# Kernel optimization log

Hardware: AMD Instinct MI355X
Metric: run time of the kernel (lower is better)

Reference implementation:

```python
import jax, jax.numpy as jnp
import numpy as np

# dims: N nodes, E edges, C channel multiplicity, NS species, RB radial basis, H radial mlp hidden
N, E, C, NS, RB, H = 4000, 128000, 128, 5, 8, 64
AVG_N = 32.0  # avg_n_neighbors


def setup_inputs() -> dict:
    key = jax.random.key(0)
    ks = jax.random.split(key, 17)
    return {
        "x_scalars": jax.random.normal(ks[0], (N, C), jnp.float32),
        "x_vectors": jax.random.normal(ks[1], (N, C, 3), jnp.float32),
        "edge_vectors": jax.random.normal(ks[2], (E, 3), jnp.float32) * 2.0,
        "radial_basis": jax.random.normal(ks[3], (E, RB), jnp.float32),
        "W1_0": jax.random.normal(ks[4], (C, C), jnp.float32),
        "W1_1": jax.random.normal(ks[5], (C, C), jnp.float32),
        "rmlp_w0": jax.random.normal(ks[6], (RB, H), jnp.float32) * np.float32(np.sqrt(4.0 / RB)),
        "rmlp_w1": jax.random.normal(ks[7], (H, H), jnp.float32) * np.float32(np.sqrt(4.0 / H)),
        "rmlp_w2": jax.random.normal(ks[8], (H, H), jnp.float32) * np.float32(np.sqrt(4.0 / H)),
        "rmlp_w3": jax.random.normal(ks[9], (H, 4 * C), jnp.float32) * np.float32(np.sqrt(1.0 / H)),
        "W2_0": jax.random.normal(ks[10], (2 * C, 2 * C), jnp.float32),
        "W2_1": jax.random.normal(ks[11], (2 * C, C), jnp.float32),
        "Wsk0": jax.random.normal(ks[12], (NS, C, 2 * C), jnp.float32),
        "Wsk1": jax.random.normal(ks[13], (NS, C, C), jnp.float32),
        "species": jax.random.randint(ks[14], (N,), 0, NS),
        "senders": jax.random.randint(ks[15], (E,), 0, N),
        "receivers": jax.random.randint(ks[16], (E,), 0, N),
    }


def reference(x_scalars, x_vectors, edge_vectors, radial_basis,
              W1_0, W1_1, rmlp_w0, rmlp_w1, rmlp_w2, rmlp_w3,
              W2_0, W2_1, Wsk0, Wsk1, species, senders, receivers):
    n_nodes = x_scalars.shape[0]
    inv_c = 1.0 / jnp.sqrt(jnp.float32(C))
    # linear_1: per-irrep channel mixing (e3nn path-normalized Linear)
    y0 = (x_scalars @ W1_0) * inv_c                                  # [N,C] 0e
    y1 = jnp.einsum('nci,cd->ndi', x_vectors, W1_1) * inv_c          # [N,C,3] 1o
    # gather to edges
    m0 = y0[senders]                                                 # [E,C]
    m1 = y1[senders]                                                 # [E,C,3]
    # spherical harmonics lmax=1, component normalization: Y0=1, Y1=sqrt(3)*unit_vec
    r = jnp.linalg.norm(edge_vectors, axis=1, keepdims=True)
    u = edge_vectors / jnp.maximum(r, 1e-12)
    Y1 = jnp.sqrt(3.0) * u                                           # [E,3]
    # tensor product filtered to 0e,1o (explicit Clebsch-Gordan, component norm)
    t0a = m0                                                         # 0e x 0e -> 0e
    t0b = jnp.einsum('eci,ei->ec', m1, Y1) / jnp.sqrt(3.0)           # 1o x 1o -> 0e
    t1a = m0[:, :, None] * Y1[:, None, :]                            # 0e x 1o -> 1o
    t1b = m1                                                         # 1o x 0e -> 1o
    # radial MLP (silu, no bias), one scalar weight per tp irrep (4C total)
    h = jax.nn.silu(radial_basis @ rmlp_w0)
    h = jax.nn.silu(h @ rmlp_w1)
    h = jax.nn.silu(h @ rmlp_w2)
    w = h @ rmlp_w3                                                  # [E,4C]
    ws0, ws1 = w[:, :C], w[:, C:2 * C]
    wv0, wv1 = w[:, 2 * C:3 * C], w[:, 3 * C:]
    scal = jnp.concatenate([t0a * ws0, t0b * ws1], axis=1)           # [E,2C]
    vec = jnp.concatenate([t1a * wv0[:, :, None], t1b * wv1[:, :, None]], axis=1)  # [E,2C,3]
    # scatter-add to receivers, neighbor normalization
    inv_nb = 1.0 / jnp.sqrt(jnp.float32(AVG_N))
    agg_s = jax.ops.segment_sum(scal, receivers, num_segments=n_nodes) * inv_nb
    agg_v = jax.ops.segment_sum(vec, receivers, num_segments=n_nodes) * inv_nb
    # linear_2: tp irreps -> (2C)x0e + Cx1o  (C output scalars + C gates)
    inv_2c = 1.0 / jnp.sqrt(jnp.float32(2 * C))
    s = (agg_s @ W2_0) * inv_2c                                      # [N,2C]
    v = jnp.einsum('nci,cd->ndi', agg_v, W2_1) * inv_2c              # [N,C,3]
    # indexed (per-species) skip connection
    s = s + jnp.einsum('nc,ncd->nd', x_scalars, Wsk0[species]) * inv_c
    v = v + jnp.einsum('nci,ncd->ndi', x_vectors, Wsk1[species]) * inv_c
    # gate: silu on scalars, silu(gates) multiplies 1o features
    out_s = jax.nn.silu(s[:, :C])
    gates = jax.nn.silu(s[:, C:])
    out_v = v * gates[:, :, None]
    return jnp.concatenate([out_s, out_v.reshape(n_nodes, 3 * C)], axis=1)  # [N,4C]
```

## Files before the change

kernel.cpp:

```cpp
#include <hip/hip_runtime.h>
#include <math.h>

#define CC 128
#define HH 64
#define RBD 8
#define WDIM 512

typedef __attribute__((ext_vector_type(8))) short short8v;
typedef __attribute__((ext_vector_type(4))) float f32x4;

__device__ __forceinline__ float silu_f(float x) {
    return x / (1.0f + __expf(-x));
}

__device__ __forceinline__ unsigned short f2bf(float x) {
    unsigned int b = __float_as_uint(x);
    unsigned int r = (b + 0x7FFFu + ((b >> 16) & 1u)) >> 16;
    return (unsigned short)r;
}

__device__ __forceinline__ float bf2f(unsigned short u) {
    return __uint_as_float(((unsigned int)u) << 16);
}

__global__ void k_prep(const float* __restrict__ w0, const float* __restrict__ w1,
                       const float* __restrict__ w2, const float* __restrict__ w3,
                       float* __restrict__ w0T, float* __restrict__ w1T,
                       float* __restrict__ w2T, float* __restrict__ w3T,
                       unsigned short* __restrict__ w3bs,
                       unsigned short* __restrict__ w0b,
                       unsigned short* __restrict__ w1b,
                       unsigned short* __restrict__ w2b) {
    int i = blockIdx.x * blockDim.x + threadIdx.x;
    if (i < 64 * 8) { int m = i / 8, k = i % 8; w0T[i] = w0[k * 64 + m]; }
    if (i < 64 * 64) { int m = i / 64, k = i % 64; w1T[i] = w1[k * 64 + m]; w2T[i] = w2[k * 64 + m]; }
    if (i < 512 * 64) { int j = i / 64, k = i % 64; w3T[i] = w3[k * 512 + j]; }
    if (i < 32768) {
        int t = i >> 10, ch = (i >> 9) & 1, lane = (i >> 3) & 63, j = i & 7;
        int k = ch * 32 + 8 * (lane >> 4) + j;
        int n = t * 16 + (lane & 15);
        w3bs[i] = f2bf(w3[k * 512 + n]);
    }
    if (i < 2048) {
        int t = i >> 9, lane = (i >> 3) & 63, j = i & 7;
        int k = 8 * (lane >> 4) + j;
        int col = t * 16 + (lane & 15);
        w0b[i] = (k < RBD) ? f2bf(w0[k * 64 + col]) : (unsigned short)0;
    }
    if (i < 4096) {
        int f = i >> 9, lane = (i >> 3) & 63, j = i & 7;
        int ks = f >> 2, t = f & 3;
        int k = ks * 32 + 8 * (lane >> 4) + j;
        int col = t * 16 + (lane & 15);
        w1b[i] = f2bf(w1[k * 64 + col]);
        w2b[i] = f2bf(w2[k * 64 + col]);
    }
}

__global__ void k_hist(const int* __restrict__ rcv, int* __restrict__ deg, int E_) {
    int e = blockIdx.x * blockDim.x + threadIdx.x;
    if (e < E_) atomicAdd(&deg[rcv[e]], 1);
}

__global__ __launch_bounds__(1024) void k_scan(const int* __restrict__ deg,
                                               int* __restrict__ off, int N) {
    __shared__ int s[1024];
    int t = threadIdx.x;
    int b = t * 4;
    int a0 = (b + 0 < N) ? deg[b + 0] : 0;
    int a1 = (b + 1 < N) ? deg[b + 1] : 0;
    int a2 = (b + 2 < N) ? deg[b + 2] : 0;
    int a3 = (b + 3 < N) ? deg[b + 3] : 0;
    int part = a0 + a1 + a2 + a3;
    s[t] = part;
    __syncthreads();
    for (int d = 1; d < 1024; d <<= 1) {
        int v = (t >= d) ? s[t - d] : 0;
        __syncthreads();
        s[t] += v;
        __syncthreads();
    }
    int excl = s[t] - part;
    if (b + 0 <= N) off[b + 0] = excl;
    if (b + 1 <= N) off[b + 1] = excl + a0;
    if (b + 2 <= N) off[b + 2] = excl + a0 + a1;
    if (b + 3 <= N) off[b + 3] = excl + a0 + a1 + a2;
}

__global__ void k_scatter(const int* __restrict__ rcv, const int* __restrict__ off,
                          int* __restrict__ cur, int* __restrict__ elist, int E_) {
    int e = blockIdx.x * blockDim.x + threadIdx.x;
    if (e < E_) {
        int r = rcv[e];
        int p = atomicAdd(&cur[r], 1);
        elist[off[r] + p] = e;
    }
}

__global__ void k_emeta(const int* __restrict__ elist, const int* __restrict__ snd,
                        const float* __restrict__ evec,
                        float4* __restrict__ up, int* __restrict__ sp, int E_) {
    int p = blockIdx.x * blockDim.x + threadIdx.x;
    if (p >= E_) return;
    int e = elist[p];
    float e0 = evec[(size_t)e * 3 + 0];
    float e1 = evec[(size_t)e * 3 + 1];
    float e2 = evec[(size_t)e * 3 + 2];
    float rn = sqrtf(e0 * e0 + e1 * e1 + e2 * e2);
    float inv = 1.0f / fmaxf(rn, 1e-12f);
    up[p] = make_float4(e0 * inv, e1 * inv, e2 * inv, 0.f);
    sp[p] = snd[e];
}

__global__ __launch_bounds__(128) void k_node_lin(
    const float* __restrict__ xs, const float* __restrict__ xv,
    const float* __restrict__ W10, const float* __restrict__ W11,
    float* __restrict__ y0, float* __restrict__ y1, int N) {
    const int d = threadIdx.x;
    const int n0 = blockIdx.x * 4;
    const int NP = N * CC;
    const float inv_c = 0.08838834764831845f;
    float a0[4] = {0.f, 0.f, 0.f, 0.f};
    float av[4][3] = {};
    #pragma unroll 4
    for (int c = 0; c < CC; c++) {
        float w10 = W10[c * CC + d];
        float w11 = W11[c * CC + d];
        #pragma unroll
        for (int n = 0; n < 4; n++) {
            a0[n] += xs[(n0 + n) * CC + c] * w10;
            #pragma unroll
            for (int i = 0; i < 3; i++)
                av[n][i] += xv[((n0 + n) * CC + c) * 3 + i] * w11;
        }
    }
    #pragma unroll
    for (int n = 0; n < 4; n++) {
        y0[(n0 + n) * CC + d] = a0[n] * inv_c;
        #pragma unroll
        for (int i = 0; i < 3; i++)
            y1[i * NP + (n0 + n) * CC + d] = av[n][i] * inv_c;
    }
}

__device__ __forceinline__ void layer64(const float4* a, float4* b,
                                        const float* __restrict__ W) {
    #pragma unroll
    for (int m = 0; m < 16; m++) {
        float s0 = 0.f, s1 = 0.f, s2 = 0.f, s3 = 0.f;
        const float* w0p = W + (4 * m + 0) * 64;
        const float* w1p = W + (4 * m + 1) * 64;
        const float* w2p = W + (4 * m + 2) * 64;
        const float* w3p = W + (4 * m + 3) * 64;
        #pragma unroll
        for (int k = 0; k < 16; k++) {
            float4 av = a[k];
            s0 += av.x * w0p[4 * k + 0] + av.y * w0p[4 * k + 1] + av.z * w0p[4 * k + 2] + av.w * w0p[4 * k + 3];
            s1 += av.x * w1p[4 * k + 0] + av.y * w1p[4 * k + 1] + av.z * w1p[4 * k + 2] + av.w * w1p[4 * k + 3];
            s2 += av.x * w2p[4 * k + 0] + av.y * w2p[4 * k + 1] + av.z * w2p[4 * k + 2] + av.w * w2p[4 * k + 3];
            s3 += av.x * w3p[4 * k + 0] + av.y * w3p[4 * k + 1] + av.z * w3p[4 * k + 2] + av.w * w3p[4 * k + 3];
        }
        b[m] = make_float4(silu_f(s0), silu_f(s1), silu_f(s2), silu_f(s3));
    }
}

__device__ __forceinline__ void mlp_body(
    const float* __restrict__ rb, int e,
    const float* __restrict__ w0T, const float* __restrict__ w1T,
    const float* __restrict__ w2T, float4* a) {
    float rbv[RBD];
    #pragma unroll
    for (int k = 0; k < RBD; k++) rbv[k] = rb[(size_t)e * RBD + k];
    float4 b[16];
    #pragma unroll
    for (int m = 0; m < 16; m++) {
        float s0 = 0.f, s1 = 0.f, s2 = 0.f, s3 = 0.f;
        #pragma unroll
        for (int k = 0; k < RBD; k++) {
            float rv = rbv[k];
            s0 += rv * w0T[(4 * m + 0) * RBD + k];
            s1 += rv * w0T[(4 * m + 1) * RBD + k];
            s2 += rv * w0T[(4 * m + 2) * RBD + k];
            s3 += rv * w0T[(4 * m + 3) * RBD + k];
        }
        a[m] = make_float4(silu_f(s0), silu_f(s1), silu_f(s2), silu_f(s3));
    }
    layer64(a, b, w1T);
    layer64(b, a, w2T);
}

__global__ __launch_bounds__(256) void k_mlpw3(
    const float* __restrict__ rb, const int* __restrict__ elist,
    const unsigned short* __restrict__ w0b, const unsigned short* __restrict__ w1b,
    const unsigned short* __restrict__ w2b, const unsigned short* __restrict__ w3bs,
    unsigned int* __restrict__ Wq, int E_) {
    const int lane = threadIdx.x & 63;
    const int wv = threadIdx.x >> 6;
    const int rbk = blockIdx.x * 4 + wv;
    const int col = lane & 15;
    const int grp = lane >> 4;

    __shared__ unsigned short hbuf[4][16][72];

    short8v a0 = (short8v){0, 0, 0, 0, 0, 0, 0, 0};
    if (grp == 0) {
        int e = elist[rbk * 16 + col];
        const float* rp = rb + (size_t)e * RBD;
        #pragma unroll
        for (int j = 0; j < RBD; j++) a0[j] = (short)f2bf(rp[j]);
    }
    f32x4 acc[4];
    {
        const unsigned short* bp = w0b + (size_t)lane * 8;
        #pragma unroll
        for (int t = 0; t < 4; t++) {
            short8v b = *(const short8v*)(bp + (size_t)t * 512);
            acc[t] = __builtin_amdgcn_mfma_f32_16x16x32_bf16(
                a0, b, (f32x4){0.f, 0.f, 0.f, 0.f}, 0, 0, 0);
        }
    }
    #pragma unroll
    for (int t = 0; t < 4; t++)
        #pragma unroll
        for (int r = 0; r < 4; r++)
            hbuf[wv][grp * 4 + r][t * 16 + col] = f2bf(silu_f(acc[t][r]));
    __syncthreads();

    {
        short8v aA = *(const short8v*)&hbuf[wv][col][8 * grp];
        short8v aB = *(const short8v*)&hbuf[wv][col][32 + 8 * grp];
        const unsigned short* bp = w1b + (size_t)lane * 8;
        #pragma unroll
        for (int t = 0; t < 4; t++) {
            short8v b0 = *(const short8v*)(bp + (size_t)(0 + t) * 512);
            short8v b1 = *(const short8v*)(bp + (size_t)(4 + t) * 512);
            f32x4 c = __builtin_amdgcn_mfma_f32_16x16x32_bf16(
                aA, b0, (f32x4){0.f, 0.f, 0.f, 0.f}, 0, 0, 0);
            acc[t] = __builtin_amdgcn_mfma_f32_16x16x32_bf16(aB, b1, c, 0, 0, 0);
        }
    }
    __syncthreads();
    #pragma unroll
    for (int t = 0; t < 4; t++)
        #pragma unroll
        for (int r = 0; r < 4; r++)
            hbuf[wv][grp * 4 + r][t * 16 + col] = f2bf(silu_f(acc[t][r]));
    __syncthreads();

    {
        short8v aA = *(const short8v*)&hbuf[wv][col][8 * grp];
        short8v aB = *(const short8v*)&hbuf[wv][col][32 + 8 * grp];
        const unsigned short* bp = w2b + (size_t)lane * 8;
        #pragma unroll
        for (int t = 0; t < 4; t++) {
            short8v b0 = *(const short8v*)(bp + (size_t)(0 + t) * 512);
            short8v b1 = *(const short8v*)(bp + (size_t)(4 + t) * 512);
            f32x4 c = __builtin_amdgcn_mfma_f32_16x16x32_bf16(
                aA, b0, (f32x4){0.f, 0.f, 0.f, 0.f}, 0, 0, 0);
            acc[t] = __builtin_amdgcn_mfma_f32_16x16x32_bf16(aB, b1, c, 0, 0, 0);
        }
    }
    __syncthreads();
    #pragma unroll
    for (int t = 0; t < 4; t++)
        #pragma unroll
        for (int r = 0; r < 4; r++)
            hbuf[wv][grp * 4 + r][t * 16 + col] = f2bf(silu_f(acc[t][r]));
    __syncthreads();

    short8v A0 = *(const short8v*)&hbuf[wv][col][8 * grp];
    short8v A1 = *(const short8v*)&hbuf[wv][col][32 + 8 * grp];

    f32x4 wacc[32];
    #pragma unroll
    for (int t = 0; t < 32; t++) wacc[t] = (f32x4){0.f, 0.f, 0.f, 0.f};

    const unsigned short* bbase = w3bs + (size_t)lane * 8;
    #pragma unroll
    for (int t = 0; t < 32; t++) {
        short8v b0 = *(const short8v*)(bbase + (size_t)(t * 2 + 0) * 512);
        short8v b1 = *(const short8v*)(bbase + (size_t)(t * 2 + 1) * 512);
        wacc[t] = __builtin_amdgcn_mfma_f32_16x16x32_bf16(A0, b0, wacc[t], 0, 0, 0);
        wacc[t] = __builtin_amdgcn_mfma_f32_16x16x32_bf16(A1, b1, wacc[t], 0, 0, 0);
    }

    const int rowq = grp * 4;
    const int jbase = rbk * 16 + rowq;
    #pragma unroll
    for (int t = 0; t < 16; t++) {
        #pragma unroll
        for (int rr = 0; rr < 4; rr++) {
            unsigned lo = f2bf(wacc[t][rr]);
            unsigned hi = f2bf(wacc[t + 16][rr]);
            Wq[(size_t)(jbase + rr) * 256 + t * 16 + col] = lo | (hi << 16);
        }
    }
}

__global__ __launch_bounds__(256, 4) void k_gather_em(
    const int* __restrict__ off, const float4* __restrict__ up,
    const int* __restrict__ sp, const unsigned int* __restrict__ Wq,
    const float* __restrict__ y0, const float* __restrict__ y1, int NP,
    float* __restrict__ agg_s, float* __restrict__ agg_v) {
    const int r = blockIdx.x;
    const int tid = threadIdx.x;
    const int half = tid >> 7;
    const int c = tid & 127;
    const int start = off[r];
    const int end = off[r + 1];

    float accs = 0.f, av0 = 0.f, av1 = 0.f, av2 = 0.f;
    const float SQ3 = 1.7320508075688772f;

    #pragma unroll 2
    for (int j = start; j < end; j++) {
        unsigned wq = Wq[(size_t)j * 256 + tid];
        float4 u = up[j];
        int s = __builtin_amdgcn_readfirstlane(sp[j]);
        float wa = bf2f((unsigned short)(wq & 0xFFFFu));
        float wb = bf2f((unsigned short)(wq >> 16));
        if (half == 0) {
            float f = y0[(size_t)s * CC + c];
            accs += f * wa;
            float bb = f * wb * SQ3;
            av0 += bb * u.x; av1 += bb * u.y; av2 += bb * u.z;
        } else {
            float f0 = y1[0 * NP + s * CC + c];
            float f1 = y1[1 * NP + s * CC + c];
            float f2 = y1[2 * NP + s * CC + c];
            accs += (f0 * u.x + f1 * u.y + f2 * u.z) * wa;
            av0 += f0 * wb; av1 += f1 * wb; av2 += f2 * wb;
        }
    }

    agg_s[(size_t)r * 256 + tid] = accs;
    float* o = agg_v + ((size_t)r * 256 + tid) * 3;
    o[0] = av0; o[1] = av1; o[2] = av2;
}

__global__ __launch_bounds__(256) void k_mlp_wp(
    const float* __restrict__ rb, const int* __restrict__ elist,
    const float* __restrict__ w0T, const float* __restrict__ w1T,
    const float* __restrict__ w2T, const float* __restrict__ w3T,
    unsigned short* __restrict__ Wp, int E_) {
    int p = blockIdx.x * blockDim.x + threadIdx.x;
    if (p >= E_) return;
    int e = elist[p];
    const int c0 = blockIdx.y * 128;

    float4 a[16];
    mlp_body(rb, e, w0T, w1T, w2T, a);

    const size_t E4 = (size_t)E_ * 4;
    for (int c = c0; c < c0 + 128; c += 8) {
        float s[8];
        #pragma unroll
        for (int q = 0; q < 8; q++) {
            const float* rp = w3T + (size_t)(c + q) * 64;
            float t0 = 0.f, t1 = 0.f, t2 = 0.f, t3 = 0.f;
            #pragma unroll
            for (int k = 0; k < 16; k++) {
                float4 h = a[k];
                t0 += h.x * rp[4 * k + 0];
                t1 += h.y * rp[4 * k + 1];
                t2 += h.z * rp[4 * k + 2];
                t3 += h.w * rp[4 * k + 3];
            }
            s[q] = (t0 + t1) + (t2 + t3);
        }
        ushort4 pk0 = make_ushort4(f2bf(s[0]), f2bf(s[1]), f2bf(s[2]), f2bf(s[3]));
        ushort4 pk1 = make_ushort4(f2bf(s[4]), f2bf(s[5]), f2bf(s[6]), f2bf(s[7]));
        *(ushort4*)(Wp + (size_t)(c >> 2) * E4 + (size_t)p * 4) = pk0;
        *(ushort4*)(Wp + (size_t)((c >> 2) + 1) * E4 + (size_t)p * 4) = pk1;
    }
}

__global__ __launch_bounds__(512, 2) void k_gather_wg(
    const int* __restrict__ off, const int* __restrict__ elist,
    const int* __restrict__ snd, const float* __restrict__ evec,
    const unsigned short* __restrict__ Wp, int E_,
    const float* __restrict__ y0, const float* __restrict__ y1, int NP,
    float* __restrict__ agg_s, float* __restrict__ agg_v) {
    const int r = blockIdx.x;
    const int tid = threadIdx.x;
    const int part = tid >> 7;
    const int c = tid & 127;

    const int start = off[r];
    const int end = off[r + 1];

    const unsigned short* __restrict__ wstream =
        Wp + (size_t)(tid >> 2) * ((size_t)E_ * 4) + (tid & 3);

    float acc0 = 0.f, acc1 = 0.f, acc2 = 0.f;
    const float SQ3 = 1.7320508075688772f;

    #pragma unroll 2
    for (int j = start; j < end; j++) {
        int e = elist[j];
        e = __builtin_amdgcn_readfirstlane(e);
        int s = snd[e];
        s = __builtin_amdgcn_readfirstlane(s);

        float e0 = evec[(size_t)e * 3 + 0];
        float e1 = evec[(size_t)e * 3 + 1];
        float e2 = evec[(size_t)e * 3 + 2];
        float rn = sqrtf(e0 * e0 + e1 * e1 + e2 * e2);
        float inv = 1.0f / fmaxf(rn, 1e-12f);
        float ux = e0 * inv, uy = e1 * inv, uz = e2 * inv;

        float w = bf2f(wstream[(size_t)j * 4]);

        if (part == 0) {
            acc0 += y0[(size_t)s * CC + c] * w;
        } else if (part == 1) {
            float f = y1[0 * NP + s * CC + c] * ux
                    + y1[1 * NP + s * CC + c] * uy
                    + y1[2 * NP + s * CC + c] * uz;
            acc0 += f * w;
        } else if (part == 2) {
            float bb = y0[(size_t)s * CC + c] * w * SQ3;
            acc0 += bb * ux; acc1 += bb * uy; acc2 += bb * uz;
        } else {
            acc0 += y1[0 * NP + s * CC + c] * w;
            acc1 += y1[1 * NP + s * CC + c] * w;
            acc2 += y1[2 * NP + s * CC + c] * w;
        }
    }

    if (part == 0) {
        agg_s[(size_t)r * 2 * CC + c] = acc0;
    } else if (part == 1) {
        agg_s[(size_t)r * 2 * CC + CC + c] = acc0;
    } else if (part == 2) {
        float* o = agg_v + ((size_t)r * 2 * CC + c) * 3;
        o[0] = acc0; o[1] = acc1; o[2] = acc2;
    } else {
        float* o = agg_v + ((size_t)r * 2 * CC + CC + c) * 3;
        o[0] = acc0; o[1] = acc1; o[2] = acc2;
    }
}

__global__ void k_mlp(const float* __restrict__ rb,
                      const float* __restrict__ w0T, const float* __restrict__ w1T,
                      const float* __restrict__ w2T,
                      float* __restrict__ h2, int E_) {
    int e = blockIdx.x * blockDim.x + threadIdx.x;
    if (e >= E_) return;
    float4 a[16];
    mlp_body(rb, e, w0T, w1T, w2T, a);
    float4* out = (float4*)(h2 + (size_t)e * HH);
    #pragma unroll
    for (int q = 0; q < 16; q++) out[q] = a[q];
}

__global__ __launch_bounds__(512, 1) void k_gather_h2(
    const int* __restrict__ off, const int* __restrict__ elist,
    const int* __restrict__ snd, const float* __restrict__ evec,
    const float* __restrict__ h2, const float* __restrict__ w3T,
    const float* __restrict__ y0, const float* __restrict__ y1, int NP,
    float* __restrict__ agg_s, float* __restrict__ agg_v) {
    const int r = blockIdx.x;
    const int tid = threadIdx.x;
    const int part = tid >> 7;
    const int c = tid & 127;

    const float4* wp = (const float4*)(w3T + (size_t)tid * 64);
    const int start = off[r];
    const int end = off[r + 1];

    float acc0 = 0.f, acc1 = 0.f, acc2 = 0.f;
    const float SQ3 = 1.7320508075688772f;

    for (int j = start; j < end; j++) {
        int e = elist[j];
        e = __builtin_amdgcn_readfirstlane(e);
        int s = snd[e];
        s = __builtin_amdgcn_readfirstlane(s);

        float e0 = evec[(size_t)e * 3 + 0];
        float e1 = evec[(size_t)e * 3 + 1];
        float e2 = evec[(size_t)e * 3 + 2];
        float rn = sqrtf(e0 * e0 + e1 * e1 + e2 * e2);
        float inv = 1.0f / fmaxf(rn, 1e-12f);
        float ux = e0 * inv, uy = e1 * inv, uz = e2 * inv;

        const float4* __restrict__ hp = (const float4*)(h2 + ((size_t)e << 6));
        float ws0 = 0.f, ws1 = 0.f, ws2 = 0.f, ws3 = 0.f;
        #pragma unroll
        for (int k = 0; k < 16; k++) {
            float4 h = hp[k];
            float4 wv = wp[k];
            ws0 += h.x * wv.x; ws1 += h.y * wv.y; ws2 += h.z * wv.z; ws3 += h.w * wv.w;
        }
        float w = (ws0 + ws1) + (ws2 + ws3);

        if (part == 0) {
            acc0 += y0[(size_t)s * CC + c] * w;
        } else if (part == 1) {
            float f = y1[0 * NP + s * CC + c] * ux
                    + y1[1 * NP + s * CC + c] * uy
                    + y1[2 * NP + s * CC + c] * uz;
            acc0 += f * w;
        } else if (part == 2) {
            float bb = y0[(size_t)s * CC + c] * w * SQ3;
            acc0 += bb * ux; acc1 += bb * uy; acc2 += bb * uz;
        } else {
            acc0 += y1[0 * NP + s * CC + c] * w;
            acc1 += y1[1 * NP + s * CC + c] * w;
            acc2 += y1[2 * NP + s * CC + c] * w;
        }
    }

    if (part == 0) {
        agg_s[(size_t)r * 2 * CC + c] = acc0;
    } else if (part == 1) {
        agg_s[(size_t)r * 2 * CC + CC + c] = acc0;
    } else if (part == 2) {
        float* o = agg_v + ((size_t)r * 2 * CC + c) * 3;
        o[0] = acc0; o[1] = acc1; o[2] = acc2;
    } else {
        float* o = agg_v + ((size_t)r * 2 * CC + CC + c) * 3;
        o[0] = acc0; o[1] = acc1; o[2] = acc2;
    }
}

__global__ __launch_bounds__(256) void k_node_out(
    const float* __restrict__ agg_s, const float* __restrict__ agg_v,
    const float* __restrict__ xs, const float* __restrict__ xv,
    const float* __restrict__ W20, const float* __restrict__ W21,
    const float* __restrict__ Wsk0, const float* __restrict__ Wsk1,
    const int* __restrict__ species,
    float* __restrict__ out, int N) {
    const int tid = threadIdx.x;
    const int n0 = blockIdx.x * 4;

    __shared__ float as_l[4 * 256];
    __shared__ float av_l[4 * 768];
    __shared__ float xs_l[4 * 128];
    __shared__ float xv_l[4 * 384];
    __shared__ float s_l[4 * 256];

    for (int i = tid; i < 4 * 256; i += 256) as_l[i] = agg_s[(size_t)n0 * 256 + i];
    for (int i = tid; i < 4 * 768; i += 256) av_l[i] = agg_v[(size_t)n0 * 768 + i];
    for (int i = tid; i < 4 * 128; i += 256) xs_l[i] = xs[(size_t)n0 * 128 + i];
    for (int i = tid; i < 4 * 384; i += 256) xv_l[i] = xv[(size_t)n0 * 384 + i];
    int sp[4];
    #pragma unroll
    for (int n = 0; n < 4; n++) sp[n] = species[n0 + n];
    __syncthreads();

    const float k_mat = 0.17677669529663687f * 0.0625f;
    const float inv_c = 0.08838834764831845f;

    {
        const int d = tid;
        float am[4] = {0.f, 0.f, 0.f, 0.f};
        for (int cc = 0; cc < 256; cc++) {
            float w = W20[cc * 256 + d];
            #pragma unroll
            for (int n = 0; n < 4; n++) am[n] += as_l[n * 256 + cc] * w;
        }
        float ak[4] = {0.f, 0.f, 0.f, 0.f};
        for (int cc = 0; cc < 128; cc++) {
            #pragma unroll
            for (int n = 0; n < 4; n++) {
                float w = Wsk0[((size_t)sp[n] * 128 + cc) * 256 + d];
                ak[n] += xs_l[n * 128 + cc] * w;
            }
        }
        #pragma unroll
        for (int n = 0; n < 4; n++) s_l[n * 256 + d] = am[n] * k_mat + ak[n] * inv_c;
    }
    __syncthreads();

    if (tid < 128) {
        #pragma unroll
        for (int n = 0; n < 4; n++)
            out[(size_t)(n0 + n) * 512 + tid] = silu_f(s_l[n * 256 + tid]);
    }

    {
        const int d = tid & 127;
        const int half = tid >> 7;
        int spB[2];
        #pragma unroll
        for (int nn = 0; nn < 2; nn++) spB[nn] = species[n0 + half * 2 + nn];

        float am[2][3] = {};
        for (int cc = 0; cc < 256; cc++) {
            float w = W21[cc * 128 + d];
            #pragma unroll
            for (int nn = 0; nn < 2; nn++) {
                int n = half * 2 + nn;
                #pragma unroll
                for (int i = 0; i < 3; i++) am[nn][i] += av_l[n * 768 + cc * 3 + i] * w;
            }
        }
        float ak[2][3] = {};
        for (int cc = 0; cc < 128; cc++) {
            #pragma unroll
            for (int nn = 0; nn < 2; nn++) {
                int n = half * 2 + nn;
                float w = Wsk1[((size_t)spB[nn] * 128 + cc) * 128 + d];
                #pragma unroll
                for (int i = 0; i < 3; i++) ak[nn][i] += xv_l[n * 384 + cc * 3 + i] * w;
            }
        }
        #pragma unroll
        for (int nn = 0; nn < 2; nn++) {
            int n = half * 2 + nn;
            float g = silu_f(s_l[n * 256 + 128 + d]);
            #pragma unroll
            for (int i = 0; i < 3; i++)
                out[(size_t)(n0 + n) * 512 + 128 + d * 3 + i] =
                    (am[nn][i] * k_mat + ak[nn][i] * inv_c) * g;
        }
    }
}

extern "C" void kernel_launch(void* const* d_in, const int* in_sizes, int n_in,
                              void* d_out, int out_size, void* d_ws, size_t ws_size,
                              hipStream_t stream) {
    const float* xs   = (const float*)d_in[0];
    const float* xv   = (const float*)d_in[1];
    const float* evec = (const float*)d_in[2];
    const float* rb   = (const float*)d_in[3];
    const float* W10  = (const float*)d_in[4];
    const float* W11  = (const float*)d_in[5];
    const float* w0   = (const float*)d_in[6];
    const float* w1   = (const float*)d_in[7];
    const float* w2   = (const float*)d_in[8];
    const float* w3   = (const float*)d_in[9];
    const float* W20  = (const float*)d_in[10];
    const float* W21  = (const float*)d_in[11];
    const float* Wsk0 = (const float*)d_in[12];
    const float* Wsk1 = (const float*)d_in[13];
    const int* species = (const int*)d_in[14];
    const int* snd = (const int*)d_in[15];
    const int* rcv = (const int*)d_in[16];

    const int N = in_sizes[0] / CC;
    const int E = in_sizes[2] / 3;
    const int NP = N * CC;

    float* ws   = (float*)d_ws;
    float* y0   = ws;
    float* y1   = y0 + (size_t)N * CC;
    float* aggs = y1 + (size_t)N * CC * 3;
    float* aggv = aggs + (size_t)N * 2 * CC;
    float* w0T  = aggv + (size_t)N * 2 * CC * 3;
    float* w1T  = w0T + 64 * 8;
    float* w2T  = w1T + 64 * 64;
    float* w3T  = w2T + 64 * 64;
    unsigned short* w3bs = (unsigned short*)(w3T + 512 * 64);
    unsigned short* w0b  = w3bs + 32768;
    unsigned short* w1b  = w0b + 2048;
    unsigned short* w2b  = w1b + 4096;
    int*   deg  = (int*)(w2b + 4096);
    int*   cur  = deg + 4096;
    int*   off  = cur + 4096;
    int*   elist = off + 4160;
    float4* up  = (float4*)(elist + E);
    int*   sp   = (int*)(up + E);
    void*  big  = (void*)(sp + E);

    size_t base_bytes = (size_t)((char*)big - (char*)d_ws);
    size_t wq_bytes   = (size_t)E * 256 * sizeof(unsigned int);
    size_t need_A = base_bytes + wq_bytes;
    size_t need_B = base_bytes + (size_t)E * WDIM * sizeof(unsigned short);

    unsigned int*   Wq  = (unsigned int*)big;
    unsigned short* Wp  = (unsigned short*)big;

    hipMemsetAsync(deg, 0, 2 * 4096 * sizeof(int), stream);
    hipLaunchKernelGGL(k_hist, dim3((E + 255) / 256), dim3(256), 0, stream, rcv, deg, E);
    hipLaunchKernelGGL(k_scan, dim3(1), dim3(1024), 0, stream, deg, off, N);
    hipLaunchKernelGGL(k_scatter, dim3((E + 255) / 256), dim3(256), 0, stream,
                       rcv, off, cur, elist, E);
    hipLaunchKernelGGL(k_prep, dim3(128), dim3(256), 0, stream,
                       w0, w1, w2, w3, w0T, w1T, w2T, w3T, w3bs, w0b, w1b, w2b);
    hipLaunchKernelGGL(k_node_lin, dim3(N / 4), dim3(128), 0, stream,
                       xs, xv, W10, W11, y0, y1, N);

    if (ws_size >= need_A && (E % 64) == 0) {
        hipLaunchKernelGGL(k_emeta, dim3((E + 255) / 256), dim3(256), 0, stream,
                           elist, snd, evec, up, sp, E);
        hipLaunchKernelGGL(k_mlpw3, dim3(E / 64), dim3(256), 0, stream,
                           rb, elist, w0b, w1b, w2b, w3bs, Wq, E);
        hipLaunchKernelGGL(k_gather_em, dim3(N), dim3(256), 0, stream,
                           off, up, sp, Wq, y0, y1, NP, aggs, aggv);
    } else if (ws_size >= need_B) {
        hipLaunchKernelGGL(k_mlp_wp, dim3((E + 255) / 256, 4), dim3(256), 0, stream,
                           rb, elist, w0T, w1T, w2T, w3T, Wp, E);
        hipLaunchKernelGGL(k_gather_wg, dim3(N), dim3(512), 0, stream,
                           off, elist, snd, evec, Wp, E, y0, y1, NP, aggs, aggv);
    } else {
        hipLaunchKernelGGL(k_mlp, dim3((E + 255) / 256), dim3(256), 0, stream,
                           rb, w0T, w1T, w2T, (float*)big, E);
        hipLaunchKernelGGL(k_gather_h2, dim3(N), dim3(512), 0, stream,
                           off, elist, snd, evec, (const float*)big, w3T,
                           y0, y1, NP, aggs, aggv);
    }

    hipLaunchKernelGGL(k_node_out, dim3(N / 4), dim3(256), 0, stream,
                       aggs, aggv, xs, xv, W20, W21, Wsk0, Wsk1, species,
                       (float*)d_out, N);
}
```

Before: 274.8 us.

## Sort nodes by species so skip-connection blocks share one weight matrix

Adds a counting sort of nodes by species (histogram, scan, scatter) and has k_node_out process species-grouped node quadruples. When all four nodes in a block share a species, one Wsk load per element serves all nodes instead of four separate loads. It also halves the nodes per block in k_node_lin to double its grid size. The cost is three extra small kernel launches, a memset, and gathered, non-contiguous row loads and stores in the output kernel.

```diff
diff --git a/kernel.cpp b/kernel.cpp
--- a/kernel.cpp
+++ b/kernel.cpp
@@ -97,6 +97,29 @@
     }
 }
 
+__global__ void k_shist(const int* __restrict__ species, int* __restrict__ scnt, int N) {
+    int i = blockIdx.x * blockDim.x + threadIdx.x;
+    if (i < N) atomicAdd(&scnt[species[i]], 1);
+}
+
+__global__ void k_sscan(const int* __restrict__ scnt, int* __restrict__ soff, int NS) {
+    if (threadIdx.x == 0) {
+        int acc = 0;
+        for (int s = 0; s < NS; s++) { soff[s] = acc; acc += scnt[s]; }
+        soff[NS] = acc;
+    }
+}
+
+__global__ void k_sscatter(const int* __restrict__ species, const int* __restrict__ soff,
+                           int* __restrict__ scur, int* __restrict__ nlist, int N) {
+    int i = blockIdx.x * blockDim.x + threadIdx.x;
+    if (i < N) {
+        int s = species[i];
+        int p = atomicAdd(&scur[s], 1);
+        nlist[soff[s] + p] = i;
+    }
+}
+
 __global__ void k_emeta(const int* __restrict__ elist, const int* __restrict__ snd,
                         const float* __restrict__ evec,
                         float4* __restrict__ up, int* __restrict__ sp, int E_) {
@@ -117,17 +140,17 @@
     const float* __restrict__ W10, const float* __restrict__ W11,
     float* __restrict__ y0, float* __restrict__ y1, int N) {
     const int d = threadIdx.x;
-    const int n0 = blockIdx.x * 4;
+    const int n0 = blockIdx.x * 2;
     const int NP = N * CC;
     const float inv_c = 0.08838834764831845f;
-    float a0[4] = {0.f, 0.f, 0.f, 0.f};
-    float av[4][3] = {};
+    float a0[2] = {0.f, 0.f};
+    float av[2][3] = {};
     #pragma unroll 4
     for (int c = 0; c < CC; c++) {
         float w10 = W10[c * CC + d];
         float w11 = W11[c * CC + d];
         #pragma unroll
-        for (int n = 0; n < 4; n++) {
+        for (int n = 0; n < 2; n++) {
             a0[n] += xs[(n0 + n) * CC + c] * w10;
             #pragma unroll
             for (int i = 0; i < 3; i++)
@@ -135,7 +158,7 @@
         }
     }
     #pragma unroll
-    for (int n = 0; n < 4; n++) {
+    for (int n = 0; n < 2; n++) {
         y0[(n0 + n) * CC + d] = a0[n] * inv_c;
         #pragma unroll
         for (int i = 0; i < 3; i++)
@@ -530,10 +553,14 @@
     const float* __restrict__ xs, const float* __restrict__ xv,
     const float* __restrict__ W20, const float* __restrict__ W21,
     const float* __restrict__ Wsk0, const float* __restrict__ Wsk1,
-    const int* __restrict__ species,
+    const int* __restrict__ nlist, const int* __restrict__ species,
     float* __restrict__ out, int N) {
     const int tid = threadIdx.x;
-    const int n0 = blockIdx.x * 4;
+    const int b0 = blockIdx.x * 4;
+    const int nid0 = nlist[min(b0 + 0, N - 1)];
+    const int nid1 = nlist[min(b0 + 1, N - 1)];
+    const int nid2 = nlist[min(b0 + 2, N - 1)];
+    const int nid3 = nlist[min(b0 + 3, N - 1)];
 
     __shared__ float as_l[4 * 256];
     __shared__ float av_l[4 * 768];
@@ -541,13 +568,33 @@
     __shared__ float xv_l[4 * 384];
     __shared__ float s_l[4 * 256];
 
-    for (int i = tid; i < 4 * 256; i += 256) as_l[i] = agg_s[(size_t)n0 * 256 + i];
-    for (int i = tid; i < 4 * 768; i += 256) av_l[i] = agg_v[(size_t)n0 * 768 + i];
-    for (int i = tid; i < 4 * 128; i += 256) xs_l[i] = xs[(size_t)n0 * 128 + i];
-    for (int i = tid; i < 4 * 384; i += 256) xv_l[i] = xv[(size_t)n0 * 384 + i];
-    int sp[4];
-    #pragma unroll
-    for (int n = 0; n < 4; n++) sp[n] = species[n0 + n];
+    {
+        as_l[0 * 256 + tid] = agg_s[(size_t)nid0 * 256 + tid];
+        as_l[1 * 256 + tid] = agg_s[(size_t)nid1 * 256 + tid];
+        as_l[2 * 256 + tid] = agg_s[(size_t)nid2 * 256 + tid];
+        as_l[3 * 256 + tid] = agg_s[(size_t)nid3 * 256 + tid];
+        for (int i = tid; i < 768; i += 256) {
+            av_l[0 * 768 + i] = agg_v[(size_t)nid0 * 768 + i];
+            av_l[1 * 768 + i] = agg_v[(size_t)nid1 * 768 + i];
+            av_l[2 * 768 + i] = agg_v[(size_t)nid2 * 768 + i];
+            av_l[3 * 768 + i] = agg_v[(size_t)nid3 * 768 + i];
+        }
+        if (tid < 128) {
+            xs_l[0 * 128 + tid] = xs[(size_t)nid0 * 128 + tid];
+            xs_l[1 * 128 + tid] = xs[(size_t)nid1 * 128 + tid];
+            xs_l[2 * 128 + tid] = xs[(size_t)nid2 * 128 + tid];
+            xs_l[3 * 128 + tid] = xs[(size_t)nid3 * 128 + tid];
+        }
+        for (int i = tid; i < 384; i += 256) {
+            xv_l[0 * 384 + i] = xv[(size_t)nid0 * 384 + i];
+            xv_l[1 * 384 + i] = xv[(size_t)nid1 * 384 + i];
+            xv_l[2 * 384 + i] = xv[(size_t)nid2 * 384 + i];
+            xv_l[3 * 384 + i] = xv[(size_t)nid3 * 384 + i];
+        }
+    }
+    const int sp0 = species[nid0], sp1 = species[nid1];
+    const int sp2 = species[nid2], sp3 = species[nid3];
+    const bool uni = (sp0 == sp1) && (sp1 == sp2) && (sp2 == sp3);
     __syncthreads();
 
     const float k_mat = 0.17677669529663687f * 0.0625f;
@@ -562,12 +609,23 @@
             for (int n = 0; n < 4; n++) am[n] += as_l[n * 256 + cc] * w;
         }
         float ak[4] = {0.f, 0.f, 0.f, 0.f};
-        for (int cc = 0; cc < 128; cc++) {
-            #pragma unroll
-            for (int n = 0; n < 4; n++) {
-                float w = Wsk0[((size_t)sp[n] * 128 + cc) * 256 + d];
-                ak[n] += xs_l[n * 128 + cc] * w;
+        if (uni) {
+            for (int cc = 0; cc < 128; cc++) {
+                float w = Wsk0[((size_t)sp0 * 128 + cc) * 256 + d];
+                #pragma unroll
+                for (int n = 0; n < 4; n++) ak[n] += xs_l[n * 128 + cc] * w;
             }
+        } else {
+            for (int cc = 0; cc < 128; cc++) {
+                float w0v = Wsk0[((size_t)sp0 * 128 + cc) * 256 + d];
+                float w1v = Wsk0[((size_t)sp1 * 128 + cc) * 256 + d];
+                float w2v = Wsk0[((size_t)sp2 * 128 + cc) * 256 + d];
+                float w3v = Wsk0[((size_t)sp3 * 128 + cc) * 256 + d];
+                ak[0] += xs_l[0 * 128 + cc] * w0v;
+                ak[1] += xs_l[1 * 128 + cc] * w1v;
+                ak[2] += xs_l[2 * 128 + cc] * w2v;
+                ak[3] += xs_l[3 * 128 + cc] * w3v;
+            }
         }
         #pragma unroll
         for (int n = 0; n < 4; n++) s_l[n * 256 + d] = am[n] * k_mat + ak[n] * inv_c;
@@ -575,46 +633,60 @@
     __syncthreads();
 
     if (tid < 128) {
-        #pragma unroll
-        for (int n = 0; n < 4; n++)
-            out[(size_t)(n0 + n) * 512 + tid] = silu_f(s_l[n * 256 + tid]);
+        out[(size_t)nid0 * 512 + tid] = silu_f(s_l[0 * 256 + tid]);
+        out[(size_t)nid1 * 512 + tid] = silu_f(s_l[1 * 256 + tid]);
+        out[(size_t)nid2 * 512 + tid] = silu_f(s_l[2 * 256 + tid]);
+        out[(size_t)nid3 * 512 + tid] = silu_f(s_l[3 * 256 + tid]);
     }
 
     {
         const int d = tid & 127;
         const int half = tid >> 7;
-        int spB[2];
-        #pragma unroll
-        for (int nn = 0; nn < 2; nn++) spB[nn] = species[n0 + half * 2 + nn];
+        const int nA = half ? nid2 : nid0;
+        const int nB = half ? nid3 : nid1;
+        const int sA = half ? sp2 : sp0;
+        const int sB = half ? sp3 : sp1;
+        const int la = half ? 2 : 0;
+        const int lb = half ? 3 : 1;
 
         float am[2][3] = {};
         for (int cc = 0; cc < 256; cc++) {
             float w = W21[cc * 128 + d];
             #pragma unroll
-            for (int nn = 0; nn < 2; nn++) {
-                int n = half * 2 + nn;
+            for (int i = 0; i < 3; i++) {
+                am[0][i] += av_l[la * 768 + cc * 3 + i] * w;
+                am[1][i] += av_l[lb * 768 + cc * 3 + i] * w;
+            }
+        }
+        float ak[2][3] = {};
+        if (uni) {
+            for (int cc = 0; cc < 128; cc++) {
+                float w = Wsk1[((size_t)sp0 * 128 + cc) * 128 + d];
                 #pragma unroll
-                for (int i = 0; i < 3; i++) am[nn][i] += av_l[n * 768 + cc * 3 + i] * w;
+                for (int i = 0; i < 3; i++) {
+                    ak[0][i] += xv_l[la * 384 + cc * 3 + i] * w;
+                    ak[1][i] += xv_l[lb * 384 + cc * 3 + i] * w;
+                }
             }
-        }
-        float ak[2][3] = {};
-        for (int cc = 0; cc < 128; cc++) {
-            #pragma unroll
-            for (int nn = 0; nn < 2; nn++) {
-                int n = half * 2 + nn;
-                float w = Wsk1[((size_t)spB[nn] * 128 + cc) * 128 + d];
+        } else {
+            for (int cc = 0; cc < 128; cc++) {
+                float wA = Wsk1[((size_t)sA * 128 + cc) * 128 + d];
+                float wB = Wsk1[((size_t)sB * 128 + cc) * 128 + d];
                 #pragma unroll
-                for (int i = 0; i < 3; i++) ak[nn][i] += xv_l[n * 384 + cc * 3 + i] * w;
+                for (int i = 0; i < 3; i++) {
+                    ak[0][i] += xv_l[la * 384 + cc * 3 + i] * wA;
+                    ak[1][i] += xv_l[lb * 384 + cc * 3 + i] * wB;
+                }
             }
         }
-        #pragma unroll
-        for (int nn = 0; nn < 2; nn++) {
-            int n = half * 2 + nn;
-            float g = silu_f(s_l[n * 256 + 128 + d]);
-            #pragma unroll
-            for (int i = 0; i < 3; i++)
-                out[(size_t)(n0 + n) * 512 + 128 + d * 3 + i] =
-                    (am[nn][i] * k_mat + ak[nn][i] * inv_c) * g;
+        float gA = silu_f(s_l[la * 256 + 128 + d]);
+        float gB = silu_f(s_l[lb * 256 + 128 + d]);
+        float* oA = out + (size_t)nA * 512 + 128 + d * 3;
+        float* oB = out + (size_t)nB * 512 + 128 + d * 3;
+        #pragma unroll
+        for (int i = 0; i < 3; i++) {
+            oA[i] = (am[0][i] * k_mat + ak[0][i] * inv_c) * gA;
+            oB[i] = (am[1][i] * k_mat + ak[1][i] * inv_c) * gB;
         }
     }
 }
@@ -643,6 +715,9 @@
     const int N = in_sizes[0] / CC;
     const int E = in_sizes[2] / 3;
     const int NP = N * CC;
+    int NS = in_sizes[12] / (CC * 2 * CC);
+    if (NS < 1) NS = 1;
+    if (NS > 63) NS = 63;
 
     float* ws   = (float*)d_ws;
     float* y0   = ws;
@@ -663,7 +738,11 @@
     int*   elist = off + 4160;
     float4* up  = (float4*)(elist + E);
     int*   sp   = (int*)(up + E);
-    void*  big  = (void*)(sp + E);
+    int*   scnt = sp + E;
+    int*   soff = scnt + 64;
+    int*   scur = soff + 65;
+    int*   nlist = scur + 127;
+    void*  big  = (void*)(nlist + N);
 
     size_t base_bytes = (size_t)((char*)big - (char*)d_ws);
     size_t wq_bytes   = (size_t)E * 256 * sizeof(unsigned int);
@@ -674,13 +753,19 @@
     unsigned short* Wp  = (unsigned short*)big;
 
     hipMemsetAsync(deg, 0, 2 * 4096 * sizeof(int), stream);
+    hipMemsetAsync(scnt, 0, 256 * sizeof(int), stream);
     hipLaunchKernelGGL(k_hist, dim3((E + 255) / 256), dim3(256), 0, stream, rcv, deg, E);
     hipLaunchKernelGGL(k_scan, dim3(1), dim3(1024), 0, stream, deg, off, N);
     hipLaunchKernelGGL(k_scatter, dim3((E + 255) / 256), dim3(256), 0, stream,
                        rcv, off, cur, elist, E);
+    hipLaunchKernelGGL(k_shist, dim3((N + 255) / 256), dim3(256), 0, stream,
+                       species, scnt, N);
+    hipLaunchKernelGGL(k_sscan, dim3(1), dim3(64), 0, stream, scnt, soff, NS);
+    hipLaunchKernelGGL(k_sscatter, dim3((N + 255) / 256), dim3(256), 0, stream,
+                       species, soff, scur, nlist, N);
     hipLaunchKernelGGL(k_prep, dim3(128), dim3(256), 0, stream,
                        w0, w1, w2, w3, w0T, w1T, w2T, w3T, w3bs, w0b, w1b, w2b);
-    hipLaunchKernelGGL(k_node_lin, dim3(N / 4), dim3(128), 0, stream,
+    hipLaunchKernelGGL(k_node_lin, dim3(N / 2), dim3(128), 0, stream,
                        xs, xv, W10, W11, y0, y1, N);
 
     if (ws_size >= need_A && (E % 64) == 0) {
@@ -703,7 +788,7 @@
                            y0, y1, NP, aggs, aggv);
     }
 
-    hipLaunchKernelGGL(k_node_out, dim3(N / 4), dim3(256), 0, stream,
-                       aggs, aggv, xs, xv, W20, W21, Wsk0, Wsk1, species,
+    hipLaunchKernelGGL(k_node_out, dim3((N + 3) / 4), dim3(256), 0, stream,
+                       aggs, aggv, xs, xv, W20, W21, Wsk0, Wsk1, nlist, species,
                        (float*)d_out, N);
 }
```

After: 311.1 us. +13.2%, slower.
